# Kernel tuning notes

Hardware: AMD Instinct MI355X
Metric: run time of the kernel (lower is better)

## Reference

```python
import jax, jax.numpy as jnp
import numpy as np

THETA = 10000.0

def _rope_cache(seq_len, d_k, dtype=jnp.float32):
    # theta_k = theta ** (-(2i/d_k)), angles[n, i] = n * theta_k[i]
    inv_freq = THETA ** (-(jnp.arange(0, d_k, 2, dtype=jnp.float32) / d_k))
    pos = jnp.arange(seq_len, dtype=jnp.float32)
    ang = pos[:, None] * inv_freq[None, :]          # [S, d_k/2]
    cos = jnp.repeat(jnp.cos(ang), 2, axis=-1)      # [S, d_k]
    sin = jnp.repeat(jnp.sin(ang), 2, axis=-1)
    return cos.astype(dtype), sin.astype(dtype)

def _apply_rope(x, cos, sin):
    # x: [..., S, d_k]; rotate even/odd pairs: rot[2i] = -x[2i+1], rot[2i+1] = x[2i]
    x2 = x.reshape(x.shape[:-1] + (x.shape[-1] // 2, 2))
    rot = jnp.stack([-x2[..., 1], x2[..., 0]], axis=-1).reshape(x.shape)
    return x * cos + rot * sin

def setup_inputs() -> dict:
    key = jax.random.key(0)
    ks = jax.random.split(key, 5)
    B, S, D = 2, 2048, 1024
    H, DK = 16, 64
    scale = (2.0 / (D + DK)) ** 0.5
    x = jax.random.normal(ks[0], (B, S, D), dtype=jnp.float32)
    Wq = jax.random.normal(ks[1], (H, D, DK), dtype=jnp.float32) * scale
    Wk = jax.random.normal(ks[2], (H, D, DK), dtype=jnp.float32) * scale
    Wv = jax.random.normal(ks[3], (H, D, DK), dtype=jnp.float32) * scale
    Wo = jax.random.normal(ks[4], (D, D), dtype=jnp.float32) * (2.0 / (2 * D)) ** 0.5
    return {"x": x, "Wq": Wq, "Wk": Wk, "Wv": Wv, "Wo": Wo}

def reference(x, Wq, Wk, Wv, Wo):
    B, S, D = x.shape
    H, _, DK = Wq.shape
    cos, sin = _rope_cache(S, DK, x.dtype)          # [S, DK]
    q = jnp.einsum('bsd,hdk->bhsk', x, Wq)
    k = jnp.einsum('bsd,hdk->bhsk', x, Wk)
    v = jnp.einsum('bsd,hdk->bhsk', x, Wv)
    q = _apply_rope(q, cos, sin)
    k = _apply_rope(k, cos, sin)
    scores = jnp.einsum('bhqk,bhsk->bhqs', q, k) / jnp.sqrt(jnp.asarray(DK, x.dtype))
    causal = jnp.tril(jnp.ones((S, S), dtype=bool))
    scores = jnp.where(causal, scores, -jnp.inf)
    attn = jax.nn.softmax(scores, axis=-1)
    out = jnp.einsum('bhqs,bhsk->bhqk', attn, v)    # [B,H,S,DK]
    out = out.transpose(0, 2, 1, 3).reshape(B, S, H * DK)  # concat heads
    return jnp.einsum('bsd,do->bso', out, Wo)
```

## Files before the change

kernel.cpp:

```cpp
#include <hip/hip_runtime.h>
#include <math.h>

typedef __attribute__((ext_vector_type(8))) short bf16x8;
typedef __attribute__((ext_vector_type(4))) float f32x4;
typedef __attribute__((ext_vector_type(16))) float f32x16;
typedef __attribute__((ext_vector_type(4))) unsigned int uint32x4;
typedef __attribute__((ext_vector_type(2))) unsigned int uint32x2;
typedef unsigned short ushort_t;
typedef unsigned int uint_t;

typedef const void __attribute__((address_space(1)))* gas_ptr;
typedef void __attribute__((address_space(3)))* las_ptr;

namespace {

constexpr int S_  = 2048;
constexpr int D_  = 1024;
constexpr float CSC = 0.18033688011f;

__device__ inline ushort_t f2bf(float f) {
    uint_t u = __builtin_bit_cast(uint_t, f);
    u += 0x7FFFu + ((u >> 16) & 1u);
    return (ushort_t)(u >> 16);
}
__device__ inline uint_t cvtpk(float lo, float hi) {
    uint_t r;
    asm("v_cvt_pk_bf16_f32 %0, %1, %2" : "=v"(r) : "v"(lo), "v"(hi));
    return r;
}
__device__ inline void plswap(uint_t& d, uint_t& s) {
    uint32x2 r = __builtin_amdgcn_permlane32_swap(d, s, false, false);
    d = r[0];
    s = r[1];
}

__device__ inline void tconv_body(const float* __restrict__ src,
                                  ushort_t* __restrict__ dst,
                                  int R, int C, int r0, int c0, int tid)
{
    __shared__ float Tl[64][65];
    #pragma unroll
    for (int l = 0; l < 4; ++l) {
        int i = tid + l * 256;
        int row = i >> 4, col = (i & 15) * 4;
        float4 v = *(const float4*)(src + (size_t)(r0 + row) * C + c0 + col);
        Tl[row][col] = v.x; Tl[row][col + 1] = v.y;
        Tl[row][col + 2] = v.z; Tl[row][col + 3] = v.w;
    }
    __syncthreads();
    #pragma unroll
    for (int l = 0; l < 4; ++l) {
        int i = tid + l * 256;
        int cc = i >> 4, rr = (i & 15) * 4;
        uint_t lo = (uint_t)f2bf(Tl[rr][cc])     | ((uint_t)f2bf(Tl[rr + 1][cc]) << 16);
        uint_t hi = (uint_t)f2bf(Tl[rr + 2][cc]) | ((uint_t)f2bf(Tl[rr + 3][cc]) << 16);
        *(uint2*)(dst + (size_t)(c0 + cc) * R + r0 + rr) = make_uint2(lo, hi);
    }
}

__global__ __launch_bounds__(256)
void prep_kernel(const float* __restrict__ x,  const float* __restrict__ Wq,
                 const float* __restrict__ Wk, const float* __restrict__ Wv,
                 const float* __restrict__ Wo,
                 ushort_t* __restrict__ xb, ushort_t* __restrict__ Wt,
                 ushort_t* __restrict__ Wot, float* __restrict__ tbl)
{
    const int b = blockIdx.x, tid = threadIdx.x;
    if (b < 2048) {
        int i = b * 256 + tid;
        float4 a = ((const float4*)x)[i * 2];
        float4 c = ((const float4*)x)[i * 2 + 1];
        uint_t u0 = (uint_t)f2bf(a.x) | ((uint_t)f2bf(a.y) << 16);
        uint_t u1 = (uint_t)f2bf(a.z) | ((uint_t)f2bf(a.w) << 16);
        uint_t u2 = (uint_t)f2bf(c.x) | ((uint_t)f2bf(c.y) << 16);
        uint_t u3 = (uint_t)f2bf(c.z) | ((uint_t)f2bf(c.w) << 16);
        ((uint4*)xb)[i] = make_uint4(u0, u1, u2, u3);
    } else if (b < 2304) {
        int i = (b - 2048) * 256 + tid;
        int s = i >> 5, p = i & 31;
        float inv = powf(10000.0f, -(float)p * (1.0f / 32.0f));
        float sn, cs;
        sincosf((float)s * inv, &sn, &cs);
        ((float2*)tbl)[i] = make_float2(cs, sn);
    } else if (b < 3072) {
        int lin = b - 2304;
        int z = lin >> 4, rx = lin & 15;
        const float* src = (z < 16 ? Wq : z < 32 ? Wk : Wv) + (size_t)(z & 15) * 65536;
        tconv_body(src, Wt + (size_t)z * 65536, 1024, 64, rx * 64, 0, tid);
    } else {
        int lin = b - 3072;
        tconv_body(Wo, Wot, 1024, 1024, (lin & 15) * 64, (lin >> 4) * 64, tid);
    }
}

template<int MODE>
__global__ __launch_bounds__(256)
void gemm_kernel(const ushort_t* __restrict__ A, const ushort_t* __restrict__ Bt,
                 ushort_t* __restrict__ Qo, ushort_t* __restrict__ Ko,
                 ushort_t* __restrict__ Vto, float* __restrict__ Co,
                 const float* __restrict__ tbl, int K)
{
    constexpr int SMEM_BYTES = (MODE == 0) ? 34816 : 16384;
    __shared__ char smem[SMEM_BYTES];
    ushort_t* As = (ushort_t*)smem;
    ushort_t* Bs = As + 4096;

    const int tid  = threadIdx.x;
    const int w    = tid >> 6, lane = tid & 63;
    const int lq   = lane & 15, lk = lane >> 4;
    const int wr   = w >> 1, wc = w & 1;
    const int m0   = blockIdx.x * 128;
    const int n0   = blockIdx.y * 128;

    f32x4 acc[4][4] = {};

    for (int k0 = 0; k0 < K; k0 += 32) {
        #pragma unroll
        for (int i = 0; i < 2; ++i) {
            int c   = i * 256 + tid;
            int row = c >> 2, c4 = c & 3;
            const ushort_t* ga = A  + (size_t)(m0 + row) * K + k0 + c4 * 8;
            const ushort_t* gb = Bt + (size_t)(n0 + row) * K + k0 + c4 * 8;
            int base = (i * 256 + w * 64) * 16;
            __builtin_amdgcn_global_load_lds((gas_ptr)ga, (las_ptr)((char*)As + base), 16, 0, 0);
            __builtin_amdgcn_global_load_lds((gas_ptr)gb, (las_ptr)((char*)Bs + base), 16, 0, 0);
        }
        __syncthreads();

        bf16x8 a[4], b[4];
        #pragma unroll
        for (int m = 0; m < 4; ++m)
            a[m] = *(const bf16x8*)((const char*)As + (wr * 64 + m * 16 + lq) * 64 + lk * 16);
        #pragma unroll
        for (int n = 0; n < 4; ++n)
            b[n] = *(const bf16x8*)((const char*)Bs + (wc * 64 + n * 16 + lq) * 64 + lk * 16);
        #pragma unroll
        for (int m = 0; m < 4; ++m)
            #pragma unroll
            for (int n = 0; n < 4; ++n)
                acc[m][n] = __builtin_amdgcn_mfma_f32_16x16x32_bf16(a[m], b[n], acc[m][n], 0, 0, 0);
        __syncthreads();
    }

    if (MODE == 0) {
        const int sel = n0 >> 10;
        ushort_t* EP = (ushort_t*)smem;
        const int h0 = (n0 & 1023) >> 6;
        if (sel < 2) {
            const float sc = (sel == 0) ? CSC : 1.0f;
            #pragma unroll
            for (int m = 0; m < 4; ++m) {
                #pragma unroll
                for (int r = 0; r < 4; ++r) {
                    int lrow = wr * 64 + m * 16 + lk * 4 + r;
                    int sG = (m0 + lrow) & 2047;
                    #pragma unroll
                    for (int n = 0; n < 4; ++n) {
                        int lcol = wc * 64 + n * 16 + lq;
                        int dk = lcol & 63;
                        float v = acc[m][n][r] * sc;
                        float2 cs = *(const float2*)(tbl + ((size_t)sG * 32 + (dk >> 1)) * 2);
                        float sp = __shfl_xor(v, 1);
                        float rv = (dk & 1) ? (v * cs.x + sp * cs.y)
                                            : (v * cs.x - sp * cs.y);
                        EP[lrow * 136 + lcol] = f2bf(rv);
                    }
                }
            }
            __syncthreads();
            ushort_t* dst = (sel == 0) ? Qo : Ko;
            #pragma unroll
            for (int it = 0; it < 8; ++it) {
                int idx = it * 256 + tid;
                int row = idx >> 4, c16 = idx & 15;
                uint4 v = *(const uint4*)(EP + row * 136 + c16 * 8);
                int mg = m0 + row;
                int b_ = mg >> 11, s = mg & 2047;
                int h = h0 + (c16 >> 3);
                int dk0 = (c16 & 7) * 8;
                *(uint4*)(dst + (((size_t)b_ * 16 + h) * 2048 + s) * 64 + dk0) = v;
            }
        } else {
            #pragma unroll
            for (int m = 0; m < 4; ++m) {
                #pragma unroll
                for (int r = 0; r < 4; ++r) {
                    int lrow = wr * 64 + m * 16 + lk * 4 + r;
                    #pragma unroll
                    for (int n = 0; n < 4; ++n) {
                        int lcol = wc * 64 + n * 16 + lq;
                        EP[lcol * 136 + lrow] = f2bf(acc[m][n][r]);
                    }
                }
            }
            __syncthreads();
            #pragma unroll
            for (int it = 0; it < 8; ++it) {
                int idx = it * 256 + tid;
                int col = idx >> 4, c16 = idx & 15;
                uint4 v = *(const uint4*)(EP + col * 136 + c16 * 8);
                int h = h0 + (col >> 6);
                int dk = col & 63;
                int sb = m0 + c16 * 8;
                int b_ = sb >> 11, s = sb & 2047;
                *(uint4*)(Vto + (((size_t)b_ * 16 + h) * 64 + dk) * 2048 + s) = v;
            }
        }
    } else {
        float* EPf = (float*)smem;
        #pragma unroll
        for (int m = 0; m < 4; ++m) {
            __syncthreads();
            #pragma unroll
            for (int r = 0; r < 4; ++r) {
                int lrow = wr * 16 + lk * 4 + r;
                #pragma unroll
                for (int n = 0; n < 4; ++n) {
                    int lcol = wc * 64 + n * 16 + lq;
                    EPf[lrow * 128 + lcol] = acc[m][n][r];
                }
            }
            __syncthreads();
            #pragma unroll
            for (int it = 0; it < 4; ++it) {
                int idx = it * 256 + tid;
                int rl = idx >> 5, c32 = idx & 31;
                float4 v = *(const float4*)(EPf + rl * 128 + c32 * 4);
                int grow = m0 + (rl >> 4) * 64 + m * 16 + (rl & 15);
                *(float4*)(Co + (size_t)grow * D_ + n0 + c32 * 4) = v;
            }
        }
    }
}

__global__ __launch_bounds__(512)
void attn_kernel(const ushort_t* __restrict__ Q, const ushort_t* __restrict__ Kg,
                 const ushort_t* __restrict__ Vt, ushort_t* __restrict__ O)
{
    __shared__ ushort_t Ks[2][128 * 64];
    __shared__ ushort_t Vs[2][64 * 128];

    const int bid = blockIdx.x;
    const int p  = 31 - (bid >> 5);
    const int bh = bid & 31;

    const int tid = threadIdx.x;
    const int w = tid >> 6, lane = tid & 63;
    const int wq = w & 1, st = w >> 1;
    const int lq = lane & 31, hi = lane >> 5;
    const size_t bhBase = (size_t)bh * S_ * 64;

    const int nt   = (p >> 1) + 1;
    const int qrel = ((p & 1) << 1) + wq;

    bf16x8 qf[4];
    {
        const ushort_t* qp = Q + bhBase + (size_t)(p * 64 + wq * 32 + lq) * 64 + hi * 8;
        qf[0] = *(const bf16x8*)(qp);
        qf[1] = *(const bf16x8*)(qp + 16);
        qf[2] = *(const bf16x8*)(qp + 32);
        qf[3] = *(const bf16x8*)(qp + 48);
    }

    const int slot0 = tid, slot1 = 512 + tid;
    const int rK0 = slot0 >> 3, rK1 = slot1 >> 3;
    const int rV0 = slot0 >> 4, rV1 = slot1 >> 4;
    const ushort_t* gk0 = Kg + bhBase + (size_t)rK0 * 64 + ((slot0 & 7) ^ (rK0 & 7)) * 8;
    const ushort_t* gk1 = Kg + bhBase + (size_t)rK1 * 64 + ((slot1 & 7) ^ (rK1 & 7)) * 8;
    const ushort_t* gv0 = Vt + bhBase + (size_t)rV0 * 2048 + ((slot0 & 15) ^ (rV0 & 7)) * 8;
    const ushort_t* gv1 = Vt + bhBase + (size_t)rV1 * 2048 + ((slot1 & 15) ^ (rV1 & 7)) * 8;

    auto stage = [&](int buf, int t) {
        const size_t ko = (size_t)t * 128 * 64;
        const size_t vo = (size_t)t * 128;
        __builtin_amdgcn_global_load_lds((gas_ptr)(gk0 + ko), (las_ptr)((char*)Ks[buf] + slot0 * 16), 16, 0, 0);
        __builtin_amdgcn_global_load_lds((gas_ptr)(gk1 + ko), (las_ptr)((char*)Ks[buf] + slot1 * 16), 16, 0, 0);
        __builtin_amdgcn_global_load_lds((gas_ptr)(gv0 + vo), (las_ptr)((char*)Vs[buf] + slot0 * 16), 16, 0, 0);
        __builtin_amdgcn_global_load_lds((gas_ptr)(gv1 + vo), (las_ptr)((char*)Vs[buf] + slot1 * 16), 16, 0, 0);
    };

    float m = -1e30f, l = 0.0f;
    f32x16 oacc[2] = {};

    const int krow = st * 32 + lq;

    stage(0, 0);

    for (int t = 0; t < nt; ++t) {
        const int cur = t & 1;
        if (t < nt - 1) {
            stage(cur ^ 1, t + 1);
            asm volatile("s_waitcnt vmcnt(4)" ::: "memory");
        } else {
            asm volatile("s_waitcnt vmcnt(0)" ::: "memory");
        }
        __builtin_amdgcn_s_barrier();
        asm volatile("" ::: "memory");

        const bool last = (t == nt - 1);
        if (!(last && st > qrel)) {
            f32x16 sacc = {};
            #pragma unroll
            for (int c = 0; c < 4; ++c) {
                int koff = krow * 128 + ((c * 32 + hi * 16) ^ ((krow & 7) << 4));
                bf16x8 kf = *(const bf16x8*)((const char*)Ks[cur] + koff);
                sacc = __builtin_amdgcn_mfma_f32_32x32x16_bf16(kf, qf[c], sacc, 0, 0, 0);
            }

            if (last && st == qrel) {
                #pragma unroll
                for (int idx = 0; idx < 16; ++idx) {
                    int kvl = (idx & 3) + 8 * (idx >> 2) + 4 * hi;
                    if (kvl > lq) sacc[idx] = -1e30f;
                }
            }

            float pm = fmaxf(sacc[0], sacc[1]);
            #pragma unroll
            for (int idx = 2; idx < 16; idx += 2)
                pm = fmaxf(fmaxf(pm, sacc[idx]), sacc[idx + 1]);
            pm = fmaxf(pm, __shfl_xor(pm, 32));

            if (__any(pm > m + 11.5f)) {
                float mn = fmaxf(m, pm);
                float al = exp2f(m - mn);
                m = mn;
                l *= al;
                #pragma unroll
                for (int idx = 0; idx < 16; ++idx) { oacc[0][idx] *= al; oacc[1][idx] *= al; }
            }

            float pv[16];
            #pragma unroll
            for (int idx = 0; idx < 16; ++idx) {
                float v = exp2f(sacc[idx] - m);
                pv[idx] = v;
                l += v;
            }

            #pragma unroll
            for (int c2 = 0; c2 < 2; ++c2) {
                uint_t w0 = cvtpk(pv[8 * c2 + 0], pv[8 * c2 + 1]);
                uint_t w1 = cvtpk(pv[8 * c2 + 2], pv[8 * c2 + 3]);
                uint_t w2 = cvtpk(pv[8 * c2 + 4], pv[8 * c2 + 5]);
                uint_t w3 = cvtpk(pv[8 * c2 + 6], pv[8 * c2 + 7]);
                plswap(w0, w2);
                plswap(w1, w3);
                uint32x4 pw; pw[0] = w0; pw[1] = w1; pw[2] = w2; pw[3] = w3;
                bf16x8 pb = __builtin_bit_cast(bf16x8, pw);
                #pragma unroll
                for (int d2 = 0; d2 < 2; ++d2) {
                    int vrow = d2 * 32 + lq;
                    int vslot = (st * 4 + c2 * 2 + hi) ^ (vrow & 7);
                    bf16x8 vf = *(const bf16x8*)((const char*)Vs[cur] + vrow * 256 + vslot * 16);
                    oacc[d2] = __builtin_amdgcn_mfma_f32_32x32x16_bf16(vf, pb, oacc[d2], 0, 0, 0);
                }
            }
        }
        asm volatile("" ::: "memory");
        __builtin_amdgcn_s_barrier();
        asm volatile("" ::: "memory");
    }

    l += __shfl_xor(l, 32);

    __syncthreads();

    float* ksf = (float*)Ks;
    float* vsf = (float*)Vs;
    const int rowi = wq * 64 + lane;
    if (st != 0) {
        float* dst = (st == 1) ? ksf : (st == 2) ? (ksf + 4096) : vsf;
        #pragma unroll
        for (int j = 0; j < 8; ++j) {
            f32x4 v4;
            v4[0] = oacc[j >> 2][(j & 3) * 4 + 0];
            v4[1] = oacc[j >> 2][(j & 3) * 4 + 1];
            v4[2] = oacc[j >> 2][(j & 3) * 4 + 2];
            v4[3] = oacc[j >> 2][(j & 3) * 4 + 3];
            *(f32x4*)(dst + rowi * 32 + ((j ^ (rowi & 7)) * 4)) = v4;
        }
        vsf[4096 + (st - 1) * 512 + rowi * 2]     = m;
        vsf[4096 + (st - 1) * 512 + rowi * 2 + 1] = l;
    }
    __syncthreads();
    if (st == 0) {
        float ms[3], ls[3];
        #pragma unroll
        for (int s2 = 0; s2 < 3; ++s2) {
            ms[s2] = vsf[4096 + s2 * 512 + rowi * 2];
            ls[s2] = vsf[4096 + s2 * 512 + rowi * 2 + 1];
        }
        float M = fmaxf(fmaxf(m, ms[0]), fmaxf(ms[1], ms[2]));
        float a0 = exp2f(m - M);
        float a1 = exp2f(ms[0] - M), a2 = exp2f(ms[1] - M), a3 = exp2f(ms[2] - M);
        float lt = a0 * l + a1 * ls[0] + a2 * ls[1] + a3 * ls[2];
        float inv = 1.0f / lt;
        const int b_ = bh >> 4, h = bh & 15;
        const int s = p * 64 + wq * 32 + lq;
        ushort_t* ob = O + ((size_t)b_ * 2048 + s) * 1024 + h * 64;
        #pragma unroll
        for (int j = 0; j < 8; ++j) {
            int soff = rowi * 32 + ((j ^ (rowi & 7)) * 4);
            f32x4 o1 = *(const f32x4*)(ksf + soff);
            f32x4 o2 = *(const f32x4*)(ksf + 4096 + soff);
            f32x4 o3 = *(const f32x4*)(vsf + soff);
            int d2 = j >> 2, base = (j & 3) * 4;
            float q0 = (a0 * oacc[d2][base + 0] + a1 * o1[0] + a2 * o2[0] + a3 * o3[0]) * inv;
            float q1 = (a0 * oacc[d2][base + 1] + a1 * o1[1] + a2 * o2[1] + a3 * o3[1]) * inv;
            float q2 = (a0 * oacc[d2][base + 2] + a1 * o1[2] + a2 * o2[2] + a3 * o3[2]) * inv;
            float q3 = (a0 * oacc[d2][base + 3] + a1 * o1[3] + a2 * o2[3] + a3 * o3[3]) * inv;
            uint2 pkv;
            pkv.x = cvtpk(q0, q1);
            pkv.y = cvtpk(q2, q3);
            *(uint2*)(ob + d2 * 32 + 8 * (j & 3) + 4 * hi) = pkv;
        }
    }
}

}

extern "C" void kernel_launch(void* const* d_in, const int* in_sizes, int n_in,
                              void* d_out, int out_size, void* d_ws, size_t ws_size,
                              hipStream_t stream)
{
    const float* x  = (const float*)d_in[0];
    const float* Wq = (const float*)d_in[1];
    const float* Wk = (const float*)d_in[2];
    const float* Wv = (const float*)d_in[3];
    const float* Wo = (const float*)d_in[4];

    ushort_t* xb  = (ushort_t*)d_ws;
    ushort_t* Wt  = xb  + 4194304;
    ushort_t* Wot = Wt  + 3145728;
    ushort_t* Qb  = Wot + 1048576;
    ushort_t* Kb  = Qb  + 4194304;
    ushort_t* Vtb = Kb  + 4194304;
    ushort_t* Ob  = Vtb + 4194304;
    float*    tbl = (float*)(Ob + 4194304);

    prep_kernel<<<3328, 256, 0, stream>>>(x, Wq, Wk, Wv, Wo, xb, Wt, Wot, tbl);

    gemm_kernel<0><<<dim3(32, 24), 256, 0, stream>>>(xb, Wt, Qb, Kb, Vtb, nullptr, tbl, 1024);

    attn_kernel<<<1024, 512, 0, stream>>>(Qb, Kb, Vtb, Ob);

    gemm_kernel<1><<<dim3(32, 8), 256, 0, stream>>>(Ob, Wot, nullptr, nullptr, nullptr,
                                                    (float*)d_out, nullptr, 1024);
}
```

Baseline: 122.3 us.

## Single-buffer attention K/V tiles and serialize split-KV merge to halve LDS

Replaces the double-buffered K/V shared-memory tiles with a single buffer, loading each tile synchronously with a full wait and an extra barrier per iteration. The final cross-wave merge changes from three partial output buffers to a single accumulator that waves add into one after another under barriers. The cross-half max and sum reductions use permlane32 swaps instead of shuffles. The aim is to cut LDS per block, possibly fitting more blocks per CU, but it gives up overlap of global loads with compute and adds barriers.

```diff
diff --git a/kernel.cpp b/kernel.cpp
--- a/kernel.cpp
+++ b/kernel.cpp
@@ -32,6 +32,16 @@
     uint32x2 r = __builtin_amdgcn_permlane32_swap(d, s, false, false);
     d = r[0];
     s = r[1];
+}
+__device__ inline float xhalf_max(float x) {
+    uint_t d = __builtin_bit_cast(uint_t, x), s = d;
+    plswap(d, s);
+    return fmaxf(__builtin_bit_cast(float, d), __builtin_bit_cast(float, s));
+}
+__device__ inline float xhalf_sum(float x) {
+    uint_t d = __builtin_bit_cast(uint_t, x), s = d;
+    plswap(d, s);
+    return __builtin_bit_cast(float, d) + __builtin_bit_cast(float, s);
 }
 
 __device__ inline void tconv_body(const float* __restrict__ src,
@@ -237,8 +247,8 @@
 void attn_kernel(const ushort_t* __restrict__ Q, const ushort_t* __restrict__ Kg,
                  const ushort_t* __restrict__ Vt, ushort_t* __restrict__ O)
 {
-    __shared__ ushort_t Ks[2][128 * 64];
-    __shared__ ushort_t Vs[2][64 * 128];
+    __shared__ ushort_t Ks[128 * 64];
+    __shared__ ushort_t Vs[64 * 128];
 
     const int bid = blockIdx.x;
     const int p  = 31 - (bid >> 5);
@@ -270,13 +280,13 @@
     const ushort_t* gv0 = Vt + bhBase + (size_t)rV0 * 2048 + ((slot0 & 15) ^ (rV0 & 7)) * 8;
     const ushort_t* gv1 = Vt + bhBase + (size_t)rV1 * 2048 + ((slot1 & 15) ^ (rV1 & 7)) * 8;
 
-    auto stage = [&](int buf, int t) {
+    auto stage = [&](int t) {
         const size_t ko = (size_t)t * 128 * 64;
         const size_t vo = (size_t)t * 128;
-        __builtin_amdgcn_global_load_lds((gas_ptr)(gk0 + ko), (las_ptr)((char*)Ks[buf] + slot0 * 16), 16, 0, 0);
-        __builtin_amdgcn_global_load_lds((gas_ptr)(gk1 + ko), (las_ptr)((char*)Ks[buf] + slot1 * 16), 16, 0, 0);
-        __builtin_amdgcn_global_load_lds((gas_ptr)(gv0 + vo), (las_ptr)((char*)Vs[buf] + slot0 * 16), 16, 0, 0);
-        __builtin_amdgcn_global_load_lds((gas_ptr)(gv1 + vo), (las_ptr)((char*)Vs[buf] + slot1 * 16), 16, 0, 0);
+        __builtin_amdgcn_global_load_lds((gas_ptr)(gk0 + ko), (las_ptr)((char*)Ks + slot0 * 16), 16, 0, 0);
+        __builtin_amdgcn_global_load_lds((gas_ptr)(gk1 + ko), (las_ptr)((char*)Ks + slot1 * 16), 16, 0, 0);
+        __builtin_amdgcn_global_load_lds((gas_ptr)(gv0 + vo), (las_ptr)((char*)Vs + slot0 * 16), 16, 0, 0);
+        __builtin_amdgcn_global_load_lds((gas_ptr)(gv1 + vo), (las_ptr)((char*)Vs + slot1 * 16), 16, 0, 0);
     };
 
     float m = -1e30f, l = 0.0f;
@@ -284,16 +294,14 @@
 
     const int krow = st * 32 + lq;
 
-    stage(0, 0);
-
     for (int t = 0; t < nt; ++t) {
-        const int cur = t & 1;
-        if (t < nt - 1) {
-            stage(cur ^ 1, t + 1);
-            asm volatile("s_waitcnt vmcnt(4)" ::: "memory");
-        } else {
-            asm volatile("s_waitcnt vmcnt(0)" ::: "memory");
-        }
+        if (t > 0) {
+            asm volatile("" ::: "memory");
+            __builtin_amdgcn_s_barrier();
+            asm volatile("" ::: "memory");
+        }
+        stage(t);
+        asm volatile("s_waitcnt vmcnt(0)" ::: "memory");
         __builtin_amdgcn_s_barrier();
         asm volatile("" ::: "memory");
 
@@ -303,7 +311,7 @@
             #pragma unroll
             for (int c = 0; c < 4; ++c) {
                 int koff = krow * 128 + ((c * 32 + hi * 16) ^ ((krow & 7) << 4));
-                bf16x8 kf = *(const bf16x8*)((const char*)Ks[cur] + koff);
+                bf16x8 kf = *(const bf16x8*)((const char*)Ks + koff);
                 sacc = __builtin_amdgcn_mfma_f32_32x32x16_bf16(kf, qf[c], sacc, 0, 0, 0);
             }
 
@@ -319,7 +327,7 @@
             #pragma unroll
             for (int idx = 2; idx < 16; idx += 2)
                 pm = fmaxf(fmaxf(pm, sacc[idx]), sacc[idx + 1]);
-            pm = fmaxf(pm, __shfl_xor(pm, 32));
+            pm = xhalf_max(pm);
 
             if (__any(pm > m + 11.5f)) {
                 float mn = fmaxf(m, pm);
@@ -352,64 +360,89 @@
                 for (int d2 = 0; d2 < 2; ++d2) {
                     int vrow = d2 * 32 + lq;
                     int vslot = (st * 4 + c2 * 2 + hi) ^ (vrow & 7);
-                    bf16x8 vf = *(const bf16x8*)((const char*)Vs[cur] + vrow * 256 + vslot * 16);
+                    bf16x8 vf = *(const bf16x8*)((const char*)Vs + vrow * 256 + vslot * 16);
                     oacc[d2] = __builtin_amdgcn_mfma_f32_32x32x16_bf16(vf, pb, oacc[d2], 0, 0, 0);
                 }
             }
         }
-        asm volatile("" ::: "memory");
-        __builtin_amdgcn_s_barrier();
-        asm volatile("" ::: "memory");
-    }
-
-    l += __shfl_xor(l, 32);
-
-    __syncthreads();
+    }
+
+    asm volatile("" ::: "memory");
+    __syncthreads();
+
+    l = xhalf_sum(l);
 
     float* ksf = (float*)Ks;
     float* vsf = (float*)Vs;
     const int rowi = wq * 64 + lane;
-    if (st != 0) {
-        float* dst = (st == 1) ? ksf : (st == 2) ? (ksf + 4096) : vsf;
+    vsf[(st * 128 + rowi) * 2 + 0] = m;
+    vsf[(st * 128 + rowi) * 2 + 1] = l;
+    __syncthreads();
+
+    float msv[4], lsv[4];
+    #pragma unroll
+    for (int i = 0; i < 4; ++i) {
+        msv[i] = vsf[(i * 128 + rowi) * 2 + 0];
+        lsv[i] = vsf[(i * 128 + rowi) * 2 + 1];
+    }
+    float M = fmaxf(fmaxf(msv[0], msv[1]), fmaxf(msv[2], msv[3]));
+    float lt = 0.0f;
+    #pragma unroll
+    for (int i = 0; i < 4; ++i) lt += exp2f(msv[i] - M) * lsv[i];
+    const float myal = exp2f(m - M);
+    const float inv  = 1.0f / lt;
+
+    if (st == 3) {
         #pragma unroll
         for (int j = 0; j < 8; ++j) {
             f32x4 v4;
-            v4[0] = oacc[j >> 2][(j & 3) * 4 + 0];
-            v4[1] = oacc[j >> 2][(j & 3) * 4 + 1];
-            v4[2] = oacc[j >> 2][(j & 3) * 4 + 2];
-            v4[3] = oacc[j >> 2][(j & 3) * 4 + 3];
-            *(f32x4*)(dst + rowi * 32 + ((j ^ (rowi & 7)) * 4)) = v4;
-        }
-        vsf[4096 + (st - 1) * 512 + rowi * 2]     = m;
-        vsf[4096 + (st - 1) * 512 + rowi * 2 + 1] = l;
+            v4[0] = myal * oacc[j >> 2][(j & 3) * 4 + 0];
+            v4[1] = myal * oacc[j >> 2][(j & 3) * 4 + 1];
+            v4[2] = myal * oacc[j >> 2][(j & 3) * 4 + 2];
+            v4[3] = myal * oacc[j >> 2][(j & 3) * 4 + 3];
+            *(f32x4*)(ksf + rowi * 32 + ((j ^ (rowi & 7)) * 4)) = v4;
+        }
+    }
+    __syncthreads();
+    if (st == 2) {
+        #pragma unroll
+        for (int j = 0; j < 8; ++j) {
+            int soff = rowi * 32 + ((j ^ (rowi & 7)) * 4);
+            f32x4 v4 = *(const f32x4*)(ksf + soff);
+            v4[0] += myal * oacc[j >> 2][(j & 3) * 4 + 0];
+            v4[1] += myal * oacc[j >> 2][(j & 3) * 4 + 1];
+            v4[2] += myal * oacc[j >> 2][(j & 3) * 4 + 2];
+            v4[3] += myal * oacc[j >> 2][(j & 3) * 4 + 3];
+            *(f32x4*)(ksf + soff) = v4;
+        }
+    }
+    __syncthreads();
+    if (st == 1) {
+        #pragma unroll
+        for (int j = 0; j < 8; ++j) {
+            int soff = rowi * 32 + ((j ^ (rowi & 7)) * 4);
+            f32x4 v4 = *(const f32x4*)(ksf + soff);
+            v4[0] += myal * oacc[j >> 2][(j & 3) * 4 + 0];
+            v4[1] += myal * oacc[j >> 2][(j & 3) * 4 + 1];
+            v4[2] += myal * oacc[j >> 2][(j & 3) * 4 + 2];
+            v4[3] += myal * oacc[j >> 2][(j & 3) * 4 + 3];
+            *(f32x4*)(ksf + soff) = v4;
+        }
     }
     __syncthreads();
     if (st == 0) {
-        float ms[3], ls[3];
-        #pragma unroll
-        for (int s2 = 0; s2 < 3; ++s2) {
-            ms[s2] = vsf[4096 + s2 * 512 + rowi * 2];
-            ls[s2] = vsf[4096 + s2 * 512 + rowi * 2 + 1];
-        }
-        float M = fmaxf(fmaxf(m, ms[0]), fmaxf(ms[1], ms[2]));
-        float a0 = exp2f(m - M);
-        float a1 = exp2f(ms[0] - M), a2 = exp2f(ms[1] - M), a3 = exp2f(ms[2] - M);
-        float lt = a0 * l + a1 * ls[0] + a2 * ls[1] + a3 * ls[2];
-        float inv = 1.0f / lt;
         const int b_ = bh >> 4, h = bh & 15;
         const int s = p * 64 + wq * 32 + lq;
         ushort_t* ob = O + ((size_t)b_ * 2048 + s) * 1024 + h * 64;
         #pragma unroll
         for (int j = 0; j < 8; ++j) {
             int soff = rowi * 32 + ((j ^ (rowi & 7)) * 4);
-            f32x4 o1 = *(const f32x4*)(ksf + soff);
-            f32x4 o2 = *(const f32x4*)(ksf + 4096 + soff);
-            f32x4 o3 = *(const f32x4*)(vsf + soff);
+            f32x4 v4 = *(const f32x4*)(ksf + soff);
             int d2 = j >> 2, base = (j & 3) * 4;
-            float q0 = (a0 * oacc[d2][base + 0] + a1 * o1[0] + a2 * o2[0] + a3 * o3[0]) * inv;
-            float q1 = (a0 * oacc[d2][base + 1] + a1 * o1[1] + a2 * o2[1] + a3 * o3[1]) * inv;
-            float q2 = (a0 * oacc[d2][base + 2] + a1 * o1[2] + a2 * o2[2] + a3 * o3[2]) * inv;
-            float q3 = (a0 * oacc[d2][base + 3] + a1 * o1[3] + a2 * o2[3] + a3 * o3[3]) * inv;
+            float q0 = (myal * oacc[d2][base + 0] + v4[0]) * inv;
+            float q1 = (myal * oacc[d2][base + 1] + v4[1]) * inv;
+            float q2 = (myal * oacc[d2][base + 2] + v4[2]) * inv;
+            float q3 = (myal * oacc[d2][base + 3] + v4[3]) * inv;
             uint2 pkv;
             pkv.x = cvtpk(q0, q1);
             pkv.y = cvtpk(q2, q3);
```

Measured after the change: 123.0 us. About the same (+0.5%).
